# Kernel optimization log

Hardware: AMD Instinct MI355X
Metric: run time of the kernel (lower is better)

The kernel has to match this reference:

```python
import jax, jax.numpy as jnp
import numpy as np

D_MODEL = 512
D_INP = 4  # freq 'h'


def setup_inputs() -> dict:
    key = jax.random.key(0)
    k1, k2, k3 = jax.random.split(key, 3)
    B, T = 32, 96
    x = jax.random.normal(k1, (B, T, D_INP), dtype=jnp.float32)
    # nn.Linear(d_inp, d_model): weight [d_model, d_inp], bias [d_model]
    W = jax.random.normal(k2, (D_MODEL, D_INP), dtype=jnp.float32) * (1.0 / np.sqrt(D_INP))
    b = jax.random.normal(k3, (D_MODEL,), dtype=jnp.float32) * 0.01
    return {"x": x, "S": 64, "W": W, "b": b}


def reference(x, S, W, b):
    # Linear embed: [B,T,d_inp] @ [d_inp,d_model] + bias -> [B,T,d_model]
    y = jnp.einsum('bte,de->btd', x, W) + b
    B, T, D = y.shape
    # Repeat each time embedding S times along a new axis -> [B,T,S,d_model]
    return jnp.broadcast_to(y[:, :, None, :], (B, T, S, D))
```

## Files before the change

kernel.cpp:

```cpp
#include <hip/hip_runtime.h>
#include <hip/hip_bf16.h>


#define D_MODEL 512
#define D_INP   4

__global__ __launch_bounds__(256) void tfe_embed_bcast(
    const float* __restrict__ x,
    const float* __restrict__ W,
    const float* __restrict__ bias,
    float* __restrict__ out,
    int S)
{
    const int bt   = blockIdx.x;
    const int tid  = threadIdx.x;
    const int d4   = tid & 127;
    const int shalf= tid >> 7;

    const float4 xv = ((const float4*)x)[bt];

    const float4* Wv = (const float4*)W;
    const float4 w0 = Wv[4 * d4 + 0];
    const float4 w1 = Wv[4 * d4 + 1];
    const float4 w2 = Wv[4 * d4 + 2];
    const float4 w3 = Wv[4 * d4 + 3];
    const float4 bv = ((const float4*)bias)[d4];

    float4 y;
    y.x = fmaf(xv.x, w0.x, fmaf(xv.y, w0.y, fmaf(xv.z, w0.z, fmaf(xv.w, w0.w, bv.x))));
    y.y = fmaf(xv.x, w1.x, fmaf(xv.y, w1.y, fmaf(xv.z, w1.z, fmaf(xv.w, w1.w, bv.y))));
    y.z = fmaf(xv.x, w2.x, fmaf(xv.y, w2.y, fmaf(xv.z, w2.z, fmaf(xv.w, w2.w, bv.z))));
    y.w = fmaf(xv.x, w3.x, fmaf(xv.y, w3.y, fmaf(xv.z, w3.z, fmaf(xv.w, w3.w, bv.w))));

    float4* orow = (float4*)out + (size_t)bt * (size_t)S * 128;
    for (int si = shalf; si < S; si += 2) {
        orow[(size_t)si * 128 + d4] = y;
    }
}

extern "C" void kernel_launch(void* const* d_in, const int* in_sizes, int n_in,
                              void* d_out, int out_size, void* d_ws, size_t ws_size,
                              hipStream_t stream) {
    const float* x    = (const float*)d_in[0];
    const float* W    = (const float*)d_in[2];
    const float* bias = (const float*)d_in[3];
    float* out        = (float*)d_out;

    const int BT = in_sizes[0] / D_INP;
    const int S  = out_size / (BT * D_MODEL);

    tfe_embed_bcast<<<BT, 256, 0, stream>>>(x, W, bias, out, S);
}
```

Before: 456.6 us.

## Add flat grid-stride broadcast kernel for power-of-two S

When S is a power of two, launches a fixed 2048-block grid-stride kernel that walks the flat output in float4 units and derives the (b,t) row from a shift. This replaces 3072 blocks that each loop over S rows, with the aim of better write-bandwidth balance across CUs. The linear projection is recomputed for every output element instead of once per thread, and each iteration reloads x from cache. The per-block kernel remains as a fallback for other S.

After: 402.7 us. 11.8% less time.

```diff
diff --git a/kernel.cpp b/kernel.cpp
--- a/kernel.cpp
+++ b/kernel.cpp
@@ -5,37 +5,58 @@
 #define D_MODEL 512
 #define D_INP   4
 
+__global__ __launch_bounds__(256) void tfe_flat(
+    const float4* __restrict__ x4,
+    const float4* __restrict__ W4,
+    const float4* __restrict__ b4,
+    float4* __restrict__ out4,
+    size_t N4, int btShift)
+{
+    const size_t stride = (size_t)gridDim.x * blockDim.x;
+    size_t f = (size_t)blockIdx.x * blockDim.x + threadIdx.x;
+    const int d4 = (int)(f & 127);
+
+    const float4 w0 = W4[4 * d4 + 0];
+    const float4 w1 = W4[4 * d4 + 1];
+    const float4 w2 = W4[4 * d4 + 2];
+    const float4 w3 = W4[4 * d4 + 3];
+    const float4 bv = b4[d4];
+
+    for (; f < N4; f += stride) {
+        const int bt = (int)(f >> btShift);
+        const float4 xv = x4[bt];
+        float4 y;
+        y.x = fmaf(xv.x, w0.x, fmaf(xv.y, w0.y, fmaf(xv.z, w0.z, fmaf(xv.w, w0.w, bv.x))));
+        y.y = fmaf(xv.x, w1.x, fmaf(xv.y, w1.y, fmaf(xv.z, w1.z, fmaf(xv.w, w1.w, bv.y))));
+        y.z = fmaf(xv.x, w2.x, fmaf(xv.y, w2.y, fmaf(xv.z, w2.z, fmaf(xv.w, w2.w, bv.z))));
+        y.w = fmaf(xv.x, w3.x, fmaf(xv.y, w3.y, fmaf(xv.z, w3.z, fmaf(xv.w, w3.w, bv.w))));
+        out4[f] = y;
+    }
+}
+
 __global__ __launch_bounds__(256) void tfe_embed_bcast(
-    const float* __restrict__ x,
-    const float* __restrict__ W,
-    const float* __restrict__ bias,
-    float* __restrict__ out,
-    int S)
+    const float* __restrict__ x, const float* __restrict__ W,
+    const float* __restrict__ bias, float* __restrict__ out, int S)
 {
-    const int bt   = blockIdx.x;
-    const int tid  = threadIdx.x;
-    const int d4   = tid & 127;
-    const int shalf= tid >> 7;
-
+    const int bt = blockIdx.x;
+    const int tid = threadIdx.x;
+    const int d4 = tid & 127;
+    const int shalf = tid >> 7;
     const float4 xv = ((const float4*)x)[bt];
-
     const float4* Wv = (const float4*)W;
     const float4 w0 = Wv[4 * d4 + 0];
     const float4 w1 = Wv[4 * d4 + 1];
     const float4 w2 = Wv[4 * d4 + 2];
     const float4 w3 = Wv[4 * d4 + 3];
     const float4 bv = ((const float4*)bias)[d4];
-
     float4 y;
     y.x = fmaf(xv.x, w0.x, fmaf(xv.y, w0.y, fmaf(xv.z, w0.z, fmaf(xv.w, w0.w, bv.x))));
     y.y = fmaf(xv.x, w1.x, fmaf(xv.y, w1.y, fmaf(xv.z, w1.z, fmaf(xv.w, w1.w, bv.y))));
     y.z = fmaf(xv.x, w2.x, fmaf(xv.y, w2.y, fmaf(xv.z, w2.z, fmaf(xv.w, w2.w, bv.z))));
     y.w = fmaf(xv.x, w3.x, fmaf(xv.y, w3.y, fmaf(xv.z, w3.z, fmaf(xv.w, w3.w, bv.w))));
-
     float4* orow = (float4*)out + (size_t)bt * (size_t)S * 128;
-    for (int si = shalf; si < S; si += 2) {
+    for (int si = shalf; si < S; si += 2)
         orow[(size_t)si * 128 + d4] = y;
-    }
 }
 
 extern "C" void kernel_launch(void* const* d_in, const int* in_sizes, int n_in,
@@ -48,6 +69,15 @@
 
     const int BT = in_sizes[0] / D_INP;
     const int S  = out_size / (BT * D_MODEL);
+    const size_t N4 = (size_t)out_size / 4;
 
-    tfe_embed_bcast<<<BT, 256, 0, stream>>>(x, W, bias, out, S);
+    if ((S & (S - 1)) == 0) {
+        int btShift = 0, v = S * (D_MODEL / 4);
+        while ((1 << (btShift + 1)) <= v) ++btShift;
+        tfe_flat<<<2048, 256, 0, stream>>>(
+            (const float4*)x, (const float4*)W, (const float4*)bias,
+            (float4*)out, N4, btShift);
+    } else {
+        tfe_embed_bcast<<<BT, 256, 0, stream>>>(x, W, bias, out, S);
+    }
 }
```
